# Kernel tuning notes

Measured on AMD Instinct MI355X. Metric: run time of the kernel, lower is better.

The kernel has to match this reference:

```python
import jax, jax.numpy as jnp
import numpy as np

ORDER = 3        # spline degree k
NUM_KNOTS = 64   # knots param from __init__


def setup_inputs() -> dict:
    key = jax.random.key(0)
    kx, kc = jax.random.split(key)
    # elementwise activation input; values outside [0,1] exercise scipy-style extrapolation
    x = jax.random.normal(kx, (4, 4096, 4096), dtype=jnp.float32)
    # nn.Parameter(torch.randn(num_knots + order))
    coefficients = jax.random.normal(kc, (NUM_KNOTS + ORDER,), dtype=jnp.float32)
    return {"x": x, "coefficients": coefficients}


def reference(x, coefficients):
    p = ORDER
    # knots = np.linspace(0, 1, num_knots + 2*order)
    t = jnp.linspace(0.0, 1.0, NUM_KNOTS + 2 * p).astype(x.dtype)
    n = t.shape[0] - p - 1  # number of basis functions scipy actually uses
    c = coefficients[:n]    # scipy ignores trailing extra coefficients

    # knot-span index; clipping to [p, n-1] reproduces extrapolate=True
    i = jnp.clip(jnp.searchsorted(t, x, side="right") - 1, p, n - 1)

    # de Boor recursion, vectorized over all elements of x
    d = [c[i - p + j] for j in range(p + 1)]  # each has shape of x
    for r in range(1, p + 1):
        for j in range(p, r - 1, -1):
            left = t[i + j - p]
            right = t[i + 1 + j - r]
            alpha = (x - left) / (right - left)
            d[j] = (1.0 - alpha) * d[j - 1] + alpha * d[j]
    return d[p]
```

## Files before the change

kernel.cpp:

```cpp
#include <hip/hip_runtime.h>

#define NCOEF 66

typedef float f32x4 __attribute__((ext_vector_type(4)));


__global__ __launch_bounds__(256) void spline_kernel(
    const float* __restrict__ x, const float* __restrict__ coef,
    float* __restrict__ out, int n)
{
    __shared__ float  sc[NCOEF];
    __shared__ float4 tab[NCOEF];

    const int t = threadIdx.x;
    if (t < NCOEF) sc[t] = coef[t];
    __syncthreads();
    if (t >= 3 && t < NCOEF) {
        float c0 = sc[t - 3], c1 = sc[t - 2], c2 = sc[t - 1], c3 = sc[t];
        const float k6 = 1.0f / 6.0f;
        float a0 = (c0 + 4.0f * c1 + c2) * k6;
        float a1 = (c2 - c0) * 0.5f;
        float a2 = (c0 - 2.0f * c1 + c2) * 0.5f;
        float a3 = (c3 - c0 + 3.0f * (c1 - c2)) * k6;
        tab[t] = make_float4(a0, a1, a2, a3);
    }
    __syncthreads();

    const int n4     = n >> 2;
    const int stride = gridDim.x * blockDim.x;
    const int gid    = blockIdx.x * blockDim.x + threadIdx.x;

    const long g = (long)gid, st = (long)stride;

    if (g + 7 * st < (long)n4 && g + 8 * st >= (long)n4) {
        const f32x4* __restrict__ xp = reinterpret_cast<const f32x4*>(x);
        f32x4*       __restrict__ op = reinterpret_cast<f32x4*>(out);

        f32x4 v[8];
        #pragma unroll
        for (int k = 0; k < 8; ++k)
            v[k] = __builtin_nontemporal_load(xp + gid + k * stride);

        #pragma unroll
        for (int k = 0; k < 8; ++k) {
            f32x4 ov;
            #pragma unroll
            for (int e = 0; e < 4; ++e) {
                float xs = v[k][e] * 69.0f;
                int   i  = (int)xs;
                i = i < 3 ? 3 : (i > 65 ? 65 : i);
                float s  = xs - (float)i;
                float4 a = tab[i];
                ov[e] = fmaf(fmaf(fmaf(a.w, s, a.z), s, a.y), s, a.x);
            }
            __builtin_nontemporal_store(ov, op + gid + k * stride);
        }
    } else {
        for (int idx = gid; idx < n4; idx += stride) {
            float4 xv = reinterpret_cast<const float4*>(x)[idx];
            float4 ov;
            #pragma unroll
            for (int e = 0; e < 4; ++e) {
                float xs = (&xv.x)[e] * 69.0f;
                int   i  = (int)xs;
                i = i < 3 ? 3 : (i > 65 ? 65 : i);
                float s  = xs - (float)i;
                float4 a = tab[i];
                (&ov.x)[e] = fmaf(fmaf(fmaf(a.w, s, a.z), s, a.y), s, a.x);
            }
            reinterpret_cast<float4*>(out)[idx] = ov;
        }
    }

    for (int k = (n4 << 2) + gid; k < n; k += stride) {
        float xs = x[k] * 69.0f;
        int   i  = (int)xs;
        i = i < 3 ? 3 : (i > 65 ? 65 : i);
        float s  = xs - (float)i;
        float4 a = tab[i];
        out[k] = fmaf(fmaf(fmaf(a.w, s, a.z), s, a.y), s, a.x);
    }
}

extern "C" void kernel_launch(void* const* d_in, const int* in_sizes, int n_in,
                              void* d_out, int out_size, void* d_ws, size_t ws_size,
                              hipStream_t stream) {
    const float* x    = (const float*)d_in[0];
    const float* coef = (const float*)d_in[1];
    float* out        = (float*)d_out;
    int n = in_sizes[0];

    int threads = 256;
    int blocks  = 8192;
    int max_blocks = ((n >> 2) + threads - 1) / threads;
    if (max_blocks < 1) max_blocks = 1;
    if (blocks > max_blocks) blocks = max_blocks;

    spline_kernel<<<blocks, threads, 0, stream>>>(x, coef, out, n);
}
```

Before: 437.5 us.

## Duplicate spline coefficient table in LDS and simplify tiled load path

Stores a second copy of the cubic coefficient table in shared memory, offset by 68 float4 entries, and has odd threads read the copy, so that lookups from adjacent lanes are meant to spread across LDS banks. Nontemporal loads and stores are replaced with ordinary vector accesses. The unrolled 8-load path now runs whenever the eighth element fits, with a remainder loop after it. The index is computed with floorf and clamped in float. This doubles the table's LDS footprint and adds a per-thread offset. Dropping the nontemporal hints may change cache behaviour for the large streaming input.

```diff
diff --git a/kernel.cpp b/kernel.cpp
--- a/kernel.cpp
+++ b/kernel.cpp
@@ -1,8 +1,7 @@
 #include <hip/hip_runtime.h>
 
 #define NCOEF 66
-
-typedef float f32x4 __attribute__((ext_vector_type(4)));
+#define TABB  (NCOEF + 2)
 
 
 __global__ __launch_bounds__(256) void spline_kernel(
@@ -10,7 +9,7 @@
     float* __restrict__ out, int n)
 {
     __shared__ float  sc[NCOEF];
-    __shared__ float4 tab[NCOEF];
+    __shared__ float4 tab[TABB + NCOEF];
 
     const int t = threadIdx.x;
     if (t < NCOEF) sc[t] = coef[t];
@@ -22,62 +21,66 @@
         float a1 = (c2 - c0) * 0.5f;
         float a2 = (c0 - 2.0f * c1 + c2) * 0.5f;
         float a3 = (c3 - c0 + 3.0f * (c1 - c2)) * k6;
-        tab[t] = make_float4(a0, a1, a2, a3);
+        float4 a = make_float4(a0, a1, a2, a3);
+        tab[t]        = a;
+        tab[TABB + t] = a;
     }
     __syncthreads();
 
     const int n4     = n >> 2;
     const int stride = gridDim.x * blockDim.x;
     const int gid    = blockIdx.x * blockDim.x + threadIdx.x;
+    const int tb     = (t & 1) ? TABB : 0;
 
-    const long g = (long)gid, st = (long)stride;
+    const float4* __restrict__ xp = reinterpret_cast<const float4*>(x);
+    float4*       __restrict__ op = reinterpret_cast<float4*>(out);
 
-    if (g + 7 * st < (long)n4 && g + 8 * st >= (long)n4) {
-        const f32x4* __restrict__ xp = reinterpret_cast<const f32x4*>(x);
-        f32x4*       __restrict__ op = reinterpret_cast<f32x4*>(out);
+    int start = gid;
 
-        f32x4 v[8];
+    if (gid + 7 * stride < n4) {
+        float4 v[8];
         #pragma unroll
         for (int k = 0; k < 8; ++k)
-            v[k] = __builtin_nontemporal_load(xp + gid + k * stride);
+            v[k] = xp[gid + k * stride];
 
         #pragma unroll
         for (int k = 0; k < 8; ++k) {
-            f32x4 ov;
-            #pragma unroll
-            for (int e = 0; e < 4; ++e) {
-                float xs = v[k][e] * 69.0f;
-                int   i  = (int)xs;
-                i = i < 3 ? 3 : (i > 65 ? 65 : i);
-                float s  = xs - (float)i;
-                float4 a = tab[i];
-                ov[e] = fmaf(fmaf(fmaf(a.w, s, a.z), s, a.y), s, a.x);
-            }
-            __builtin_nontemporal_store(ov, op + gid + k * stride);
-        }
-    } else {
-        for (int idx = gid; idx < n4; idx += stride) {
-            float4 xv = reinterpret_cast<const float4*>(x)[idx];
             float4 ov;
             #pragma unroll
             for (int e = 0; e < 4; ++e) {
-                float xs = (&xv.x)[e] * 69.0f;
-                int   i  = (int)xs;
-                i = i < 3 ? 3 : (i > 65 ? 65 : i);
-                float s  = xs - (float)i;
-                float4 a = tab[i];
+                float xs = (&v[k].x)[e] * 69.0f;
+                float fi = floorf(xs);
+                fi = fi < 3.0f ? 3.0f : (fi > 65.0f ? 65.0f : fi);
+                float s  = xs - fi;
+                float4 a = tab[tb + (int)fi];
                 (&ov.x)[e] = fmaf(fmaf(fmaf(a.w, s, a.z), s, a.y), s, a.x);
             }
-            reinterpret_cast<float4*>(out)[idx] = ov;
+            op[gid + k * stride] = ov;
         }
+        start = gid + 8 * stride;
+    }
+
+    for (int idx = start; idx < n4; idx += stride) {
+        float4 xv = xp[idx];
+        float4 ov;
+        #pragma unroll
+        for (int e = 0; e < 4; ++e) {
+            float xs = (&xv.x)[e] * 69.0f;
+            float fi = floorf(xs);
+            fi = fi < 3.0f ? 3.0f : (fi > 65.0f ? 65.0f : fi);
+            float s  = xs - fi;
+            float4 a = tab[tb + (int)fi];
+            (&ov.x)[e] = fmaf(fmaf(fmaf(a.w, s, a.z), s, a.y), s, a.x);
+        }
+        op[idx] = ov;
     }
 
     for (int k = (n4 << 2) + gid; k < n; k += stride) {
         float xs = x[k] * 69.0f;
-        int   i  = (int)xs;
-        i = i < 3 ? 3 : (i > 65 ? 65 : i);
-        float s  = xs - (float)i;
-        float4 a = tab[i];
+        float fi = floorf(xs);
+        fi = fi < 3.0f ? 3.0f : (fi > 65.0f ? 65.0f : fi);
+        float s  = xs - fi;
+        float4 a = tab[tb + (int)fi];
         out[k] = fmaf(fmaf(fmaf(a.w, s, a.z), s, a.y), s, a.x);
     }
 }
```

Result: no change. 431.1 us (-1.5%).
